# Kernel tuning notes

Measured on AMD Instinct MI355X. Metric: run time of the kernel, lower is better.

Reference implementation:

```python
import jax, jax.numpy as jnp
from jax import lax
import numpy as np
import math

N_HEAD = 8
MAX_REL = 16


def _layer_norm(x, g, b, eps=1e-5):
    mu = jnp.mean(x, -1, keepdims=True)
    var = jnp.var(x, -1, keepdims=True)
    return (x - mu) / jnp.sqrt(var + eps) * g + b


def _pos_encoding(S, H):
    # PositionalEncoding buffer: row 0 is zeros, rows 1..para_limit are sin/cos of positions 0..para_limit-1
    pe = np.zeros((1001, H), np.float32)
    pos = np.arange(0, 1000, dtype=np.float32)[:, None]
    div = np.exp(np.arange(0, H, 2, dtype=np.float32) * (-math.log(10000.0) / H))
    pe[1:, 0::2] = np.sin(pos * div)
    pe[1:, 1::2] = np.cos(pos * div)
    return jnp.asarray(pe[:S])


def setup_inputs() -> dict:
    key = jax.random.key(0)
    B, S, H, NC, K = 32, 512, 512, 2, 7
    NH, M = N_HEAD, MAX_REL
    dk = H // NH
    V = 2 * M + 1
    ks = jax.random.split(key, 16)
    sd = 0.02
    f32 = jnp.float32
    return {
        "x": jax.random.normal(ks[0], (B, S, H), f32),
        "mask": jnp.ones((B, S), jnp.int32),
        # conv blocks (stacked over NC)
        "dw_w": (jax.random.normal(ks[1], (NC, H, 1, K), f32) * sd),
        "dw_b": jnp.zeros((NC, H), f32),
        "pw_w": (jax.random.normal(ks[2], (NC, H, H), f32) * sd),
        "pw_b": jnp.zeros((NC, H), f32),
        "ln_conv_g": jnp.ones((NC, H), f32),
        "ln_conv_b": jnp.zeros((NC, H), f32),
        # attention (torch Linear convention: W is (out,in))
        "wq": jax.random.normal(ks[3], (H, H), f32) * sd,
        "bq": jnp.zeros((H,), f32),
        "wk": jax.random.normal(ks[4], (H, H), f32) * sd,
        "bk": jnp.zeros((H,), f32),
        "wv": jax.random.normal(ks[5], (H, H), f32) * sd,
        "bv": jnp.zeros((H,), f32),
        "wo": jax.random.normal(ks[6], (H, H), f32) * sd,
        "bo": jnp.zeros((H,), f32),
        "embed_k": jax.random.normal(ks[7], (V, dk), f32) * sd,
        "embed_v": jax.random.normal(ks[8], (V, dk), f32) * sd,
        "ln_att_g": jnp.ones((H,), f32),
        "ln_att_b": jnp.zeros((H,), f32),
        # feed-forward block (hidden->hidden)
        "w_ff": jax.random.normal(ks[9], (H, H), f32) * sd,
        "b_ff": jnp.zeros((H,), f32),
        "ln_ffn_g": jnp.ones((H,), f32),
        "ln_ffn_b": jnp.zeros((H,), f32),
    }


def reference(x, mask, dw_w, dw_b, pw_w, pw_b, ln_conv_g, ln_conv_b,
              wq, bq, wk, bk, wv, bv, wo, bo, embed_k, embed_v,
              ln_att_g, ln_att_b, w_ff, b_ff, ln_ffn_g, ln_ffn_b):
    B, S, H = x.shape
    NH = N_HEAD
    dk = H // NH
    M = MAX_REL
    NC = dw_w.shape[0]
    K = dw_w.shape[-1]

    # positional encoding (scale_fact = 1)
    x = x + _pos_encoding(S, H)[None] * mask[..., None].astype(x.dtype)

    # conv blocks: x + relu(pointwise(depthwise(LN(x))))
    for i in range(NC):
        n = _layer_norm(x, ln_conv_g[i], ln_conv_b[i])
        h = n.transpose(0, 2, 1)  # (B,H,S)
        h = lax.conv_general_dilated(
            h, dw_w[i], window_strides=(1,), padding=[(K // 2, K // 2)],
            dimension_numbers=("NCH", "OIH", "NCH"), feature_group_count=H,
        ) + dw_b[i][None, :, None]
        h = jnp.einsum("bcs,oc->bos", h, pw_w[i]) + pw_b[i][None, :, None]
        h = jax.nn.relu(h).transpose(0, 2, 1)
        x = x + h

    # self-attention block with relative position representations (Shaw et al.)
    n = _layer_norm(x, ln_att_g, ln_att_b)
    q = (jnp.einsum("bsh,oh->bso", n, wq) + bq).reshape(B, S, NH, dk).transpose(0, 2, 1, 3)
    k = (jnp.einsum("bsh,oh->bso", n, wk) + bk).reshape(B, S, NH, dk).transpose(0, 2, 1, 3)
    v = (jnp.einsum("bsh,oh->bso", n, wv) + bv).reshape(B, S, NH, dk).transpose(0, 2, 1, 3)

    pos = jnp.arange(S)
    idx = jnp.clip(pos[None, :] - pos[:, None], -M, M) + M  # (S,S)
    rel_k = embed_k[idx]  # (S,S,dk)
    rel_v = embed_v[idx]  # (S,S,dk)

    # NOTE: original code applies no 1/sqrt(dk) scaling and effectively uses plain softmax
    logits = jnp.einsum("bhqd,bhkd->bhqk", q, k) + jnp.einsum("bhqd,qkd->bhqk", q, rel_k)
    w = jax.nn.softmax(logits, axis=-1)
    o = jnp.einsum("bhqk,bhkd->bhqd", w, v) + jnp.einsum("bhqk,qkd->bhqd", w, rel_v)
    o = o.transpose(0, 2, 1, 3).reshape(B, S, H)
    x = x + jnp.einsum("bsh,oh->bso", o, wo) + bo

    # feed-forward block: x + relu(Linear(LN(x)))
    n = _layer_norm(x, ln_ffn_g, ln_ffn_b)
    x = x + jax.nn.relu(jnp.einsum("bsh,oh->bso", n, w_ff) + b_ff)
    return x
```

## Files before the change

### kernel.cpp

```cpp
#include <hip/hip_runtime.h>

#define SEQ 512
#define HD 512
#define BATCH 32
#define TOK (BATCH * SEQ)
#define NHEAD 8
#define DKDIM 64
#define MREL 16
#define NRELV 33

using short8 = __attribute__((ext_vector_type(8))) short;
using f32x4  = __attribute__((ext_vector_type(4))) float;
using f32x16 = __attribute__((ext_vector_type(16))) float;
typedef unsigned short ushortT;

#define AS1 __attribute__((address_space(1)))
#define AS3 __attribute__((address_space(3)))
#define GLDS16(g, l) __builtin_amdgcn_global_load_lds( \
    (const AS1 unsigned int*)(const void*)(g), \
    (AS3 unsigned int*)(void*)(l), 16, 0, 0)

__device__ __forceinline__ ushortT f2bf(float x) {
  union { float f; unsigned u; } c; c.f = x;
  unsigned r = c.u + 0x7FFF + ((c.u >> 16) & 1);
  return (ushortT)(r >> 16);
}

__device__ __forceinline__ float bf2f(ushortT h) {
  union { unsigned u; float f; } c; c.u = (unsigned)h << 16;
  return c.f;
}

__global__ __launch_bounds__(256) void pe_kernel(float* __restrict__ PE) {
  const int i = blockIdx.x * 256 + threadIdx.x;
  const int s = i >> 9, h = i & (HD - 1);
  float v = 0.f;
  if (s > 0) {
    const int i2 = h & ~1;
    const float div = expf((float)i2 * (-9.210340371976184f / (float)HD));
    const float ang = (float)(s - 1) * div;
    v = (h & 1) ? cosf(ang) : sinf(ang);
  }
  PE[i] = v;
}

__global__ __launch_bounds__(256) void convw_kernel(
    const float* __restrict__ s0, const float* __restrict__ s1,
    const float* __restrict__ s2, const float* __restrict__ s3,
    const float* __restrict__ s4, const float* __restrict__ s5,
    const float* __restrict__ s6, ushortT* __restrict__ dst) {
  const int i = blockIdx.x * 256 + threadIdx.x;
  const int region = i >> 16;
  const int off = i & 65535;
  const float* s = region == 0 ? s0 : region == 1 ? s1 : region == 2 ? s2 :
                   region == 3 ? s3 : region == 4 ? s4 : region == 5 ? s5 : s6;
  const float4 v = ((const float4*)s)[off];
  ushort4 o;
  o.x = f2bf(v.x); o.y = f2bf(v.y); o.z = f2bf(v.z); o.w = f2bf(v.w);
  *(ushort4*)&dst[(long)i * 4] = o;
}

__global__ __launch_bounds__(256) void addpos_ln_kernel(
    const float* __restrict__ X, const int* __restrict__ mask,
    const float* __restrict__ PE, const float* __restrict__ g,
    const float* __restrict__ bta, float* __restrict__ out,
    ushortT* __restrict__ Y) {
  const int row = blockIdx.x;
  const int t = threadIdx.x;
  const int s0i = row & (SEQ - 1);
  const float mk = (float)mask[row];
  const float x0 = X[(long)row * HD + t]       + PE[s0i * HD + t] * mk;
  const float x1 = X[(long)row * HD + t + 256] + PE[s0i * HD + t + 256] * mk;
  out[(long)row * HD + t] = x0;
  out[(long)row * HD + t + 256] = x1;
  float s = x0 + x1, q = x0 * x0 + x1 * x1;
  #pragma unroll
  for (int off = 32; off > 0; off >>= 1) {
    s += __shfl_down(s, off);
    q += __shfl_down(q, off);
  }
  __shared__ float sh[10];
  const int w = t >> 6;
  if ((t & 63) == 0) { sh[w] = s; sh[4 + w] = q; }
  __syncthreads();
  if (t == 0) {
    const float S_ = sh[0] + sh[1] + sh[2] + sh[3];
    const float Q_ = sh[4] + sh[5] + sh[6] + sh[7];
    const float mu = S_ * (1.f / (float)HD);
    const float var = Q_ * (1.f / (float)HD) - mu * mu;
    sh[8] = mu;
    sh[9] = rsqrtf(var + 1e-5f);
  }
  __syncthreads();
  const float mu = sh[8], rstd = sh[9];
  ushortT* yr = Y + (long)row * HD;
  yr[t]       = f2bf((x0 - mu) * rstd * g[t] + bta[t]);
  yr[t + 256] = f2bf((x1 - mu) * rstd * g[t + 256] + bta[t + 256]);
}

template <bool BF>
__global__ __launch_bounds__(256) void ln_kernel(
    const float* __restrict__ X, const float* __restrict__ g,
    const float* __restrict__ bta, void* __restrict__ Yv) {
  const int row = blockIdx.x;
  const int t = threadIdx.x;
  const float* xr = X + (long)row * HD;
  const float x0 = xr[t], x1 = xr[t + 256];
  float s = x0 + x1, q = x0 * x0 + x1 * x1;
  #pragma unroll
  for (int off = 32; off > 0; off >>= 1) {
    s += __shfl_down(s, off);
    q += __shfl_down(q, off);
  }
  __shared__ float sh[10];
  const int w = t >> 6;
  if ((t & 63) == 0) { sh[w] = s; sh[4 + w] = q; }
  __syncthreads();
  if (t == 0) {
    const float S_ = sh[0] + sh[1] + sh[2] + sh[3];
    const float Q_ = sh[4] + sh[5] + sh[6] + sh[7];
    const float mu = S_ * (1.f / (float)HD);
    const float var = Q_ * (1.f / (float)HD) - mu * mu;
    sh[8] = mu;
    sh[9] = rsqrtf(var + 1e-5f);
  }
  __syncthreads();
  const float mu = sh[8], rstd = sh[9];
  const float y0 = (x0 - mu) * rstd * g[t] + bta[t];
  const float y1 = (x1 - mu) * rstd * g[t + 256] + bta[t + 256];
  if (BF) {
    ushortT* yr = (ushortT*)Yv + (long)row * HD;
    yr[t] = f2bf(y0);
    yr[t + 256] = f2bf(y1);
  } else {
    float* yr = (float*)Yv + (long)row * HD;
    yr[t] = y0;
    yr[t + 256] = y1;
  }
}

__global__ __launch_bounds__(256) void dwconv_kernel(
    const ushortT* __restrict__ N_, const float* __restrict__ w,
    const float* __restrict__ bias, ushortT* __restrict__ Hout) {
  const int t = threadIdx.x;
  const int cg = t & 63, sb = t >> 6;
  const int tile = blockIdx.x;
  const int b = tile >> 5;
  const int s0 = ((tile & 31) << 4) + (sb << 2);
  const long rowb = (long)b * SEQ;
  const int c0 = cg * 8;

  float wr[56];
  #pragma unroll
  for (int i = 0; i < 14; ++i) {
    const float4 v = *(const float4*)&w[c0 * 7 + i * 4];
    wr[i * 4 + 0] = v.x; wr[i * 4 + 1] = v.y;
    wr[i * 4 + 2] = v.z; wr[i * 4 + 3] = v.w;
  }
  float bz[8];
  #pragma unroll
  for (int i = 0; i < 2; ++i) {
    const float4 v = *(const float4*)&bias[c0 + i * 4];
    bz[i * 4 + 0] = v.x; bz[i * 4 + 1] = v.y;
    bz[i * 4 + 2] = v.z; bz[i * 4 + 3] = v.w;
  }

  const short8 zero = {};
  short8 win[7];
  #pragma unroll
  for (int k = 0; k < 7; ++k) {
    const int ss = s0 + k - 3;
    win[k] = (ss >= 0 && ss < SEQ) ? *(const short8*)&N_[(rowb + ss) * HD + c0] : zero;
  }
  #pragma unroll
  for (int u = 0; u < 4; ++u) {
    float acc[8];
    #pragma unroll
    for (int j = 0; j < 8; ++j) acc[j] = bz[j];
    #pragma unroll
    for (int k = 0; k < 7; ++k)
      #pragma unroll
      for (int j = 0; j < 8; ++j)
        acc[j] += bf2f((ushortT)win[k][j]) * wr[j * 7 + k];
    short8 o;
    #pragma unroll
    for (int j = 0; j < 8; ++j) o[j] = (short)f2bf(acc[j]);
    *(short8*)&Hout[(rowb + s0 + u) * HD + c0] = o;
    if (u < 3) {
      #pragma unroll
      for (int k = 0; k < 6; ++k) win[k] = win[k + 1];
      const int ss = s0 + u + 4;
      win[6] = (ss < SEQ) ? *(const short8*)&N_[(rowb + ss) * HD + c0] : zero;
    }
  }
}

__device__ __forceinline__ void gemm_tile512(
    const ushortT* __restrict__ A, const ushortT* __restrict__ W,
    int row0, int col0, int t, ushortT* Als, ushortT* Bls, f32x4 acc[4][2]) {
  const int lane = t & 63, w = t >> 6;
  const int wr = w >> 2, wc = w & 3;
  const int l15 = lane & 15, lhi = lane >> 4;
  for (int kt = 0; kt < 8; ++kt) {
    __syncthreads();
    #pragma unroll
    for (int i = 0; i < 2; ++i) {
      const int tl = i * 512 + t;
      const int r = tl >> 3, sl = tl & 7;
      const int sc = sl ^ (r & 7);
      GLDS16(A + (long)(row0 + r) * HD + kt * 64 + sc * 8,
             Als + (i * 512 + w * 64) * 8);
      GLDS16(W + (long)(col0 + r) * HD + kt * 64 + sc * 8,
             Bls + (i * 512 + w * 64) * 8);
    }
    __syncthreads();
    #pragma unroll
    for (int kk = 0; kk < 2; ++kk) {
      short8 af[4], bf[2];
      #pragma unroll
      for (int i = 0; i < 4; ++i) {
        const int ra = wr * 64 + i * 16 + l15;
        af[i] = *(const short8*)&Als[ra * 64 + (((kk * 4 + lhi) ^ (ra & 7)) << 3)];
      }
      #pragma unroll
      for (int j = 0; j < 2; ++j) {
        const int rb = wc * 32 + j * 16 + l15;
        bf[j] = *(const short8*)&Bls[rb * 64 + (((kk * 4 + lhi) ^ (rb & 7)) << 3)];
      }
      #pragma unroll
      for (int mi = 0; mi < 4; ++mi)
        #pragma unroll
        for (int ni = 0; ni < 2; ++ni)
          acc[mi][ni] = __builtin_amdgcn_mfma_f32_16x16x32_bf16(af[mi], bf[ni], acc[mi][ni], 0, 0, 0);
    }
  }
}

template <int MODE>
__global__ __launch_bounds__(512) void mgemm512_kernel(
    const ushortT* __restrict__ A, const ushortT* __restrict__ W,
    const float* __restrict__ bias, float* __restrict__ C,
    ushortT* __restrict__ Cb) {
  __shared__ ushortT Als[128 * 64];
  __shared__ ushortT Bls[128 * 64];
  const int t = threadIdx.x;
  const int bid = blockIdx.x;
  const int m_blk = (bid & 7) * 16 + ((bid >> 3) & 15);
  const int n_blk = bid >> 7;
  const int row0 = m_blk * 128, col0 = n_blk * 128;
  const int lane = t & 63, w = t >> 6;
  const int wr = w >> 2, wc = w & 3;
  const int l15 = lane & 15, lhi = lane >> 4;

  f32x4 acc[4][2] = {};
  gemm_tile512(A, W, row0, col0, t, Als, Bls, acc);

  #pragma unroll
  for (int ni = 0; ni < 2; ++ni) {
    const int c = col0 + wc * 32 + ni * 16 + l15;
    const float bz = bias[c];
    #pragma unroll
    for (int mi = 0; mi < 4; ++mi) {
      #pragma unroll
      for (int reg = 0; reg < 4; ++reg) {
        const int rrow = row0 + wr * 64 + mi * 16 + lhi * 4 + reg;
        const float g = acc[mi][ni][reg] + bz;
        const long idx = (long)rrow * HD + c;
        if (MODE == 0)      C[idx] = g;
        else if (MODE == 1) C[idx] += g;
        else if (MODE == 2) C[idx] += fmaxf(g, 0.f);
        else                Cb[idx] = f2bf(g);
      }
    }
  }
}

__global__ __launch_bounds__(512) void qkv_kernel(
    const ushortT* __restrict__ A, const ushortT* __restrict__ Wbase,
    const float* __restrict__ bq, const float* __restrict__ bk,
    const float* __restrict__ bv, ushortT* __restrict__ Q,
    ushortT* __restrict__ K, ushortT* __restrict__ Vt) {
  __shared__ ushortT Als[128 * 64];
  __shared__ ushortT Bls[128 * 64];
  const int t = threadIdx.x;
  const int z = blockIdx.y;
  const ushortT* W = Wbase + (long)z * HD * HD;
  const float* bias = z == 0 ? bq : z == 1 ? bk : bv;
  const int bid = blockIdx.x;
  const int m_blk = (bid & 7) * 16 + ((bid >> 3) & 15);
  const int n_blk = bid >> 7;
  const int row0 = m_blk * 128, col0 = n_blk * 128;
  const int lane = t & 63, w = t >> 6;
  const int wr = w >> 2, wc = w & 3;
  const int l15 = lane & 15, lhi = lane >> 4;

  f32x4 acc[4][2] = {};
  gemm_tile512(A, W, row0, col0, t, Als, Bls, acc);

  #pragma unroll
  for (int ni = 0; ni < 2; ++ni) {
    const int c = col0 + wc * 32 + ni * 16 + l15;
    const float bz = bias[c];
    #pragma unroll
    for (int mi = 0; mi < 4; ++mi) {
      if (z == 2) {
        const int tok0 = row0 + wr * 64 + mi * 16 + lhi * 4;
        const int b = tok0 >> 9, s0 = tok0 & (SEQ - 1);
        const int hh2 = c >> 6, dd = c & 63;
        ushort4 pk;
        pk.x = f2bf(acc[mi][ni][0] + bz);
        pk.y = f2bf(acc[mi][ni][1] + bz);
        pk.z = f2bf(acc[mi][ni][2] + bz);
        pk.w = f2bf(acc[mi][ni][3] + bz);
        const long off = ((((long)(b * NHEAD + hh2) * 16 + (s0 >> 5)) * 4 +
                           ((s0 & 31) >> 3)) * 2 + (dd >> 5)) * 256 +
                         (dd & 31) * 8 + (s0 & 7);
        *(ushort4*)&Vt[off] = pk;
      } else {
        ushortT* Cb = (z == 0) ? Q : K;
        const int hh2 = c >> 6, dd = c & 63;
        #pragma unroll
        for (int reg = 0; reg < 4; ++reg) {
          const int rrow = row0 + wr * 64 + mi * 16 + lhi * 4 + reg;
          const int b = rrow >> 9, s = rrow & (SEQ - 1);
          const long off = ((((long)(b * NHEAD + hh2) * 16 + (s >> 5)) * 4 +
                             (dd >> 4)) * 2 + ((dd >> 3) & 1)) * 256 +
                           (s & 31) * 8 + (dd & 7);
          Cb[off] = f2bf(acc[mi][ni][reg] + bz);
        }
      }
    }
  }
}

__global__ __launch_bounds__(512, 4) void attn_kernel(
    const ushortT* __restrict__ Qf, const ushortT* __restrict__ Kf,
    const ushortT* __restrict__ Vf, const float* __restrict__ ekg,
    const float* __restrict__ evg, ushortT* __restrict__ Og) {
  __shared__ ushortT qekL[8][32][34];
  __shared__ ushortT wsAll[8][32][56];
  __shared__ ushortT EVT[64][56];
  __shared__ float LROWw[8][32];
  __shared__ float WHIw[8][32];

  const int t = threadIdx.x;
  const int lane = t & 63, w = t >> 6;
  const int l31 = lane & 31, h = lane >> 5;
  const int hh = blockIdx.x, qb = blockIdx.y, bb = blockIdx.z;
  const int q0w = qb * 256 + w * 32;
  const long qkb = ((long)bb * SEQ) * HD + hh * DKDIM;
  const long fbase = (long)(bb * NHEAD + hh) * 16;

  for (int i = t; i < 64 * 56; i += 512) {
    const int d = i / 56, r = i % 56;
    EVT[d][r] = (r < NRELV) ? f2bf(evg[r * 64 + d]) : (ushortT)0;
  }
  {
    unsigned* wz = (unsigned*)&wsAll[w][0][0];
    #pragma unroll
    for (int i = 0; i < 14; ++i) wz[lane + i * 64] = 0u;
  }
  __syncthreads();

  short8 qB[4];
  #pragma unroll
  for (int kk = 0; kk < 4; ++kk)
    qB[kk] = *(const short8*)&Qf[(((fbase + qb * 8 + w) * 4 + kk) * 2 + h) * 256 + l31 * 8];

  {
    f32x16 qacc = {};
    #pragma unroll
    for (int kk = 0; kk < 4; ++kk) {
      short8 ef;
      #pragma unroll
      for (int j = 0; j < 8; ++j)
        ef[j] = (short)f2bf(ekg[l31 * 64 + kk * 16 + h * 8 + j]);
      qacc = __builtin_amdgcn_mfma_f32_32x32x16_bf16(ef, qB[kk], qacc, 0, 0, 0);
    }
    #pragma unroll
    for (int r = 0; r < 16; ++r) {
      const int rr = (r & 3) + 8 * (r >> 2) + 4 * h;
      qekL[w][l31][rr] = f2bf(qacc[r]);
    }
  }
  float qekHiR = 0.f, qekLoR = 0.f;
  #pragma unroll
  for (int kk = 0; kk < 4; ++kk)
    #pragma unroll
    for (int j = 0; j < 8; ++j) {
      const float qv = bf2f((ushortT)qB[kk][j]);
      const int d = kk * 16 + h * 8 + j;
      qekHiR += qv * ekg[32 * 64 + d];
      qekLoR += qv * ekg[d];
    }
  qekHiR += __shfl_xor(qekHiR, 32);
  qekLoR += __shfl_xor(qekLoR, 32);
  if (h == 0) qekL[w][l31][32] = f2bf(qekHiR);

  const int qg = q0w + l31;
  f32x16 oaccL = {}, oaccH = {};
  float rsum = 0.f, wsHi = 0.f;

  for (int kt = 0; kt < 16; ++kt) {
    const int k0 = kt * 32;
    f32x16 sacc = {};
    __builtin_amdgcn_s_setprio(1);
    #pragma unroll
    for (int kk = 0; kk < 4; ++kk) {
      const short8 kf = *(const short8*)&Kf[(((fbase + kt) * 4 + kk) * 2 + h) * 256 + l31 * 8];
      sacc = __builtin_amdgcn_mfma_f32_32x32x16_bf16(kf, qB[kk], sacc, 0, 0, 0);
    }
    __builtin_amdgcn_s_setprio(0);
    const int dmin = k0 - q0w - 31, dmax = k0 + 31 - q0w;
    if (dmin >= MREL) {
      #pragma unroll
      for (int r = 0; r < 16; ++r) {
        const float p = __expf(sacc[r] + qekHiR);
        sacc[r] = p; rsum += p; wsHi += p;
      }
    } else if (dmax <= -MREL) {
      #pragma unroll
      for (int r = 0; r < 16; ++r) {
        const float p = __expf(sacc[r] + qekLoR);
        sacc[r] = p; rsum += p;
      }
    } else {
      #pragma unroll
      for (int r = 0; r < 16; ++r) {
        const int key = k0 + (r & 3) + 8 * (r >> 2) + 4 * h;
        const int db = key - qg;
        const int rcl = min(max(db, -MREL), MREL) + MREL;
        const float p = __expf(sacc[r] + bf2f(qekL[w][l31][rcl]));
        sacc[r] = p; rsum += p;
        if (db >= MREL)       wsHi += p;
        else if (db > -MREL)  wsAll[w][l31][db + MREL] = f2bf(p);
      }
    }
    #pragma unroll
    for (int c = 0; c < 2; ++c) {
      const int rb = c * 8;
      unsigned a0, a1, b0, b1;
      asm("v_cvt_pk_bf16_f32 %0, %1, %2" : "=v"(a0) : "v"(sacc[rb + 0]), "v"(sacc[rb + 1]));
      asm("v_cvt_pk_bf16_f32 %0, %1, %2" : "=v"(a1) : "v"(sacc[rb + 2]), "v"(sacc[rb + 3]));
      asm("v_cvt_pk_bf16_f32 %0, %1, %2" : "=v"(b0) : "v"(sacc[rb + 4]), "v"(sacc[rb + 5]));
      asm("v_cvt_pk_bf16_f32 %0, %1, %2" : "=v"(b1) : "v"(sacc[rb + 6]), "v"(sacc[rb + 7]));
      asm("v_permlane32_swap_b32 %0, %1" : "+v"(a0), "+v"(b0));
      asm("v_permlane32_swap_b32 %0, %1" : "+v"(a1), "+v"(b1));
      union { unsigned u[4]; short8 s; } pa;
      pa.u[0] = a0; pa.u[1] = a1; pa.u[2] = b0; pa.u[3] = b1;
      const short8 v0 = *(const short8*)&Vf[((((fbase + kt) * 4 + c * 2 + h) * 2 + 0) * 256) + l31 * 8];
      const short8 v1 = *(const short8*)&Vf[((((fbase + kt) * 4 + c * 2 + h) * 2 + 1) * 256) + l31 * 8];
      __builtin_amdgcn_s_setprio(1);
      oaccL = __builtin_amdgcn_mfma_f32_32x32x16_bf16(pa.s, v0, oaccL, 0, 0, 0);
      oaccH = __builtin_amdgcn_mfma_f32_32x32x16_bf16(pa.s, v1, oaccH, 0, 0, 0);
      __builtin_amdgcn_s_setprio(0);
    }
  }

  rsum += __shfl_xor(rsum, 32);
  wsHi += __shfl_xor(wsHi, 32);
  if (h == 0) { LROWw[w][l31] = rsum; WHIw[w][l31] = wsHi; }

  if (h == 0) {
    float ms = 0.f;
    #pragma unroll
    for (int cch = 0; cch < 4; ++cch) {
      const short8 v = *(const short8*)&wsAll[w][l31][cch * 8];
      #pragma unroll
      for (int j = 0; j < 8; ++j) ms += bf2f((ushortT)v[j]);
    }
    wsAll[w][l31][0]  = f2bf(rsum - wsHi - ms);
    wsAll[w][l31][32] = f2bf(wsHi);
  }

  #pragma unroll
  for (int kk = 0; kk < 3; ++kk) {
    const short8 aw = *(const short8*)&wsAll[w][l31][kk * 16 + h * 8];
    const short8 bL = *(const short8*)&EVT[l31][kk * 16 + h * 8];
    const short8 bH = *(const short8*)&EVT[l31 + 32][kk * 16 + h * 8];
    oaccL = __builtin_amdgcn_mfma_f32_32x32x16_bf16(aw, bL, oaccL, 0, 0, 0);
    oaccH = __builtin_amdgcn_mfma_f32_32x32x16_bf16(aw, bH, oaccH, 0, 0, 0);
  }

  const int dl = l31;
  #pragma unroll
  for (int r = 0; r < 16; ++r) {
    const int qr = (r & 3) + 8 * (r >> 2) + 4 * h;
    const float rinv = 1.f / LROWw[w][qr];
    const long orow = qkb + (long)(q0w + qr) * HD;
    Og[orow + dl] = f2bf(oaccL[r] * rinv);
    Og[orow + dl + 32] = f2bf(oaccH[r] * rinv);
  }
}

extern "C" void kernel_launch(void* const* d_in, const int* in_sizes, int n_in,
                              void* d_out, int out_size, void* d_ws, size_t ws_size,
                              hipStream_t stream) {
  const float* x    = (const float*)d_in[0];
  const int*   mask = (const int*)d_in[1];
  const float* dw_w = (const float*)d_in[2];
  const float* dw_b = (const float*)d_in[3];
  const float* pw_w = (const float*)d_in[4];
  const float* pw_b = (const float*)d_in[5];
  const float* lncg = (const float*)d_in[6];
  const float* lncb = (const float*)d_in[7];
  const float* wq   = (const float*)d_in[8];
  const float* bq   = (const float*)d_in[9];
  const float* wk   = (const float*)d_in[10];
  const float* bk   = (const float*)d_in[11];
  const float* wv   = (const float*)d_in[12];
  const float* bv   = (const float*)d_in[13];
  const float* wo   = (const float*)d_in[14];
  const float* bo   = (const float*)d_in[15];
  const float* ek   = (const float*)d_in[16];
  const float* ev   = (const float*)d_in[17];
  const float* lnag = (const float*)d_in[18];
  const float* lnab = (const float*)d_in[19];
  const float* wff  = (const float*)d_in[20];
  const float* bff  = (const float*)d_in[21];
  const float* lnfg = (const float*)d_in[22];
  const float* lnfb = (const float*)d_in[23];

  float* out = (float*)d_out;
  float* PE   = (float*)d_ws;
  float* NB32 = PE + SEQ * HD;
  ushortT* ABF = (ushortT*)(NB32 + (long)TOK * HD);
  ushortT* QBF = ABF + (long)TOK * HD;
  ushortT* KBF = QBF + (long)TOK * HD;
  ushortT* VTB = KBF + (long)TOK * HD;
  ushortT* WBF = VTB + (long)TOK * HD;
  const long WSZ = (long)HD * HD;

  pe_kernel<<<SEQ * HD / 256, 256, 0, stream>>>(PE);
  convw_kernel<<<7 * HD * HD / 4 / 256, 256, 0, stream>>>(
      pw_w, pw_w + WSZ, wq, wk, wv, wo, wff, WBF);
  addpos_ln_kernel<<<TOK, 256, 0, stream>>>(x, mask, PE, lncg, lncb, out, QBF);

  dwconv_kernel<<<BATCH * SEQ / 16, 256, 0, stream>>>(QBF, dw_w, dw_b, ABF);
  mgemm512_kernel<2><<<512, 512, 0, stream>>>(ABF, WBF, pw_b, out, nullptr);

  ln_kernel<true><<<TOK, 256, 0, stream>>>(out, lncg + HD, lncb + HD, QBF);
  dwconv_kernel<<<BATCH * SEQ / 16, 256, 0, stream>>>(QBF, dw_w + HD * 7, dw_b + HD, ABF);
  mgemm512_kernel<2><<<512, 512, 0, stream>>>(ABF, WBF + WSZ, pw_b + HD, out, nullptr);

  ln_kernel<true><<<TOK, 256, 0, stream>>>(out, lnag, lnab, ABF);
  qkv_kernel<<<dim3(512, 3), 512, 0, stream>>>(ABF, WBF + 2 * WSZ, bq, bk, bv, QBF, KBF, VTB);
  attn_kernel<<<dim3(NHEAD, SEQ / 256, BATCH), 512, 0, stream>>>(QBF, KBF, VTB, ek, ev, ABF);
  mgemm512_kernel<1><<<512, 512, 0, stream>>>(ABF, WBF + 5 * WSZ, bo, out, nullptr);

  ln_kernel<true><<<TOK, 256, 0, stream>>>(out, lnfg, lnfb, ABF);
  mgemm512_kernel<2><<<512, 512, 0, stream>>>(ABF, WBF + 6 * WSZ, bff, out, nullptr);
}
```

Baseline: 245.0 us.

## Compute softmax row sums via MFMA with ones, prefetch K fragments, merge init kernels

```diff
diff --git a/kernel.cpp b/kernel.cpp
--- a/kernel.cpp
+++ b/kernel.cpp
@@ -31,33 +31,36 @@
   return c.f;
 }
 
-__global__ __launch_bounds__(256) void pe_kernel(float* __restrict__ PE) {
-  const int i = blockIdx.x * 256 + threadIdx.x;
-  const int s = i >> 9, h = i & (HD - 1);
-  float v = 0.f;
-  if (s > 0) {
-    const int i2 = h & ~1;
-    const float div = expf((float)i2 * (-9.210340371976184f / (float)HD));
-    const float ang = (float)(s - 1) * div;
-    v = (h & 1) ? cosf(ang) : sinf(ang);
-  }
-  PE[i] = v;
-}
-
-__global__ __launch_bounds__(256) void convw_kernel(
+__global__ __launch_bounds__(256) void init_kernel(
+    float* __restrict__ PE,
     const float* __restrict__ s0, const float* __restrict__ s1,
     const float* __restrict__ s2, const float* __restrict__ s3,
     const float* __restrict__ s4, const float* __restrict__ s5,
     const float* __restrict__ s6, ushortT* __restrict__ dst) {
-  const int i = blockIdx.x * 256 + threadIdx.x;
-  const int region = i >> 16;
-  const int off = i & 65535;
-  const float* s = region == 0 ? s0 : region == 1 ? s1 : region == 2 ? s2 :
-                   region == 3 ? s3 : region == 4 ? s4 : region == 5 ? s5 : s6;
-  const float4 v = ((const float4*)s)[off];
-  ushort4 o;
-  o.x = f2bf(v.x); o.y = f2bf(v.y); o.z = f2bf(v.z); o.w = f2bf(v.w);
-  *(ushort4*)&dst[(long)i * 4] = o;
+  const int b = blockIdx.x;
+  const int t = threadIdx.x;
+  if (b < SEQ * HD / 256) {
+    const int i = b * 256 + t;
+    const int s = i >> 9, h = i & (HD - 1);
+    float v = 0.f;
+    if (s > 0) {
+      const int i2 = h & ~1;
+      const float div = expf((float)i2 * (-9.210340371976184f / (float)HD));
+      const float ang = (float)(s - 1) * div;
+      v = (h & 1) ? cosf(ang) : sinf(ang);
+    }
+    PE[i] = v;
+  } else {
+    const int i = (b - SEQ * HD / 256) * 256 + t;
+    const int region = i >> 16;
+    const int off = i & 65535;
+    const float* s = region == 0 ? s0 : region == 1 ? s1 : region == 2 ? s2 :
+                     region == 3 ? s3 : region == 4 ? s4 : region == 5 ? s5 : s6;
+    const float4 v = ((const float4*)s)[off];
+    ushort4 o;
+    o.x = f2bf(v.x); o.y = f2bf(v.y); o.z = f2bf(v.z); o.w = f2bf(v.w);
+    *(ushort4*)&dst[(long)i * 4] = o;
+  }
 }
 
 __global__ __launch_bounds__(256) void addpos_ln_kernel(
@@ -398,32 +401,42 @@
   if (h == 0) qekL[w][l31][32] = f2bf(qekHiR);
 
   const int qg = q0w + l31;
-  f32x16 oaccL = {}, oaccH = {};
-  float rsum = 0.f, wsHi = 0.f;
+  f32x16 oaccL = {}, oaccH = {}, oaccR = {}, oaccHi = {};
+  float wsHiS = 0.f;
+  short8 ones;
+  #pragma unroll
+  for (int j = 0; j < 8; ++j) ones[j] = (short)0x3F80;
+
+  short8 kf[4];
+  #pragma unroll
+  for (int kk = 0; kk < 4; ++kk)
+    kf[kk] = *(const short8*)&Kf[((fbase * 4 + kk) * 2 + h) * 256 + l31 * 8];
 
   for (int kt = 0; kt < 16; ++kt) {
     const int k0 = kt * 32;
     f32x16 sacc = {};
     __builtin_amdgcn_s_setprio(1);
     #pragma unroll
-    for (int kk = 0; kk < 4; ++kk) {
-      const short8 kf = *(const short8*)&Kf[(((fbase + kt) * 4 + kk) * 2 + h) * 256 + l31 * 8];
-      sacc = __builtin_amdgcn_mfma_f32_32x32x16_bf16(kf, qB[kk], sacc, 0, 0, 0);
-    }
+    for (int kk = 0; kk < 4; ++kk)
+      sacc = __builtin_amdgcn_mfma_f32_32x32x16_bf16(kf[kk], qB[kk], sacc, 0, 0, 0);
     __builtin_amdgcn_s_setprio(0);
+
+    const int ktn = (kt < 15) ? kt + 1 : 15;
+    short8 kfn[4];
+    #pragma unroll
+    for (int kk = 0; kk < 4; ++kk)
+      kfn[kk] = *(const short8*)&Kf[(((fbase + ktn) * 4 + kk) * 2 + h) * 256 + l31 * 8];
+
     const int dmin = k0 - q0w - 31, dmax = k0 + 31 - q0w;
-    if (dmin >= MREL) {
-      #pragma unroll
-      for (int r = 0; r < 16; ++r) {
-        const float p = __expf(sacc[r] + qekHiR);
-        sacc[r] = p; rsum += p; wsHi += p;
-      }
+    const bool uniHi = (dmin >= MREL);
+    if (uniHi) {
+      #pragma unroll
+      for (int r = 0; r < 16; ++r)
+        sacc[r] = __expf(sacc[r] + qekHiR);
     } else if (dmax <= -MREL) {
       #pragma unroll
-      for (int r = 0; r < 16; ++r) {
-        const float p = __expf(sacc[r] + qekLoR);
-        sacc[r] = p; rsum += p;
-      }
+      for (int r = 0; r < 16; ++r)
+        sacc[r] = __expf(sacc[r] + qekLoR);
     } else {
       #pragma unroll
       for (int r = 0; r < 16; ++r) {
@@ -431,8 +444,8 @@
         const int db = key - qg;
         const int rcl = min(max(db, -MREL), MREL) + MREL;
         const float p = __expf(sacc[r] + bf2f(qekL[w][l31][rcl]));
-        sacc[r] = p; rsum += p;
-        if (db >= MREL)       wsHi += p;
+        sacc[r] = p;
+        if (db >= MREL)       wsHiS += p;
         else if (db > -MREL)  wsAll[w][l31][db + MREL] = f2bf(p);
       }
     }
@@ -453,14 +466,25 @@
       __builtin_amdgcn_s_setprio(1);
       oaccL = __builtin_amdgcn_mfma_f32_32x32x16_bf16(pa.s, v0, oaccL, 0, 0, 0);
       oaccH = __builtin_amdgcn_mfma_f32_32x32x16_bf16(pa.s, v1, oaccH, 0, 0, 0);
+      oaccR = __builtin_amdgcn_mfma_f32_32x32x16_bf16(pa.s, ones, oaccR, 0, 0, 0);
+      if (uniHi)
+        oaccHi = __builtin_amdgcn_mfma_f32_32x32x16_bf16(pa.s, ones, oaccHi, 0, 0, 0);
       __builtin_amdgcn_s_setprio(0);
     }
-  }
-
-  rsum += __shfl_xor(rsum, 32);
-  wsHi += __shfl_xor(wsHi, 32);
-  if (h == 0) { LROWw[w][l31] = rsum; WHIw[w][l31] = wsHi; }
-
+    #pragma unroll
+    for (int kk = 0; kk < 4; ++kk) kf[kk] = kfn[kk];
+  }
+
+  wsHiS += __shfl_xor(wsHiS, 32);
+  if (l31 == 0) {
+    #pragma unroll
+    for (int r = 0; r < 16; ++r) {
+      const int qr = (r & 3) + 8 * (r >> 2) + 4 * h;
+      LROWw[w][qr] = oaccR[r];
+      WHIw[w][qr]  = oaccHi[r];
+    }
+  }
+  if (h == 0) WHIw[w][l31] += wsHiS;
   if (h == 0) {
     float ms = 0.f;
     #pragma unroll
@@ -469,8 +493,8 @@
       #pragma unroll
       for (int j = 0; j < 8; ++j) ms += bf2f((ushortT)v[j]);
     }
-    wsAll[w][l31][0]  = f2bf(rsum - wsHi - ms);
-    wsAll[w][l31][32] = f2bf(wsHi);
+    wsAll[w][l31][0]  = f2bf(LROWw[w][l31] - WHIw[w][l31] - ms);
+    wsAll[w][l31][32] = f2bf(WHIw[w][l31]);
   }
 
   #pragma unroll
@@ -486,7 +510,7 @@
   #pragma unroll
   for (int r = 0; r < 16; ++r) {
     const int qr = (r & 3) + 8 * (r >> 2) + 4 * h;
-    const float rinv = 1.f / LROWw[w][qr];
+    const float rinv = 1.f / oaccR[r];
     const long orow = qkb + (long)(q0w + qr) * HD;
     Og[orow + dl] = f2bf(oaccL[r] * rinv);
     Og[orow + dl + 32] = f2bf(oaccH[r] * rinv);
@@ -531,9 +555,8 @@
   ushortT* WBF = VTB + (long)TOK * HD;
   const long WSZ = (long)HD * HD;
 
-  pe_kernel<<<SEQ * HD / 256, 256, 0, stream>>>(PE);
-  convw_kernel<<<7 * HD * HD / 4 / 256, 256, 0, stream>>>(
-      pw_w, pw_w + WSZ, wq, wk, wv, wo, wff, WBF);
+  init_kernel<<<SEQ * HD / 256 + 7 * HD * HD / 4 / 256, 256, 0, stream>>>(
+      PE, pw_w, pw_w + WSZ, wq, wk, wv, wo, wff, WBF);
   addpos_ln_kernel<<<TOK, 256, 0, stream>>>(x, mask, PE, lncg, lncb, out, QBF);
 
   dwconv_kernel<<<BATCH * SEQ / 16, 256, 0, stream>>>(QBF, dw_w, dw_b, ABF);
```

Result: slower. 266.2 us (+8.6%).
